# Optimization experiments

Hardware: AMD Instinct MI355X
Metric: run time of the kernel (lower is better)

## Reference

```python
import jax, jax.numpy as jnp
import numpy as np

N = 100000
E = 3200000
IN_DIM = 128
HID = 16
OUT = 2


def setup_inputs() -> dict:
    key = jax.random.key(0)
    k_x, k_e, k_w1, k_w2 = jax.random.split(key, 4)
    x = jax.random.normal(k_x, (N, IN_DIM), dtype=jnp.float32)
    edge_index = jax.random.randint(k_e, (2, E), 0, N, dtype=jnp.int64)
    # Glorot-style init like PyG GCNConv
    W1 = jax.random.normal(k_w1, (IN_DIM, HID), dtype=jnp.float32) * (1.0 / np.sqrt(IN_DIM))
    b1 = jnp.zeros((HID,), dtype=jnp.float32)
    W2 = jax.random.normal(k_w2, (HID, OUT), dtype=jnp.float32) * (1.0 / np.sqrt(HID))
    b2 = jnp.zeros((OUT,), dtype=jnp.float32)
    return {"x": x, "edge_index": edge_index, "W1": W1, "b1": b1, "W2": W2, "b2": b2}


def _gcn_conv(x, src, dst, norm, W, b):
    # PyG GCNConv: linear transform first, then normalized scatter-add, then bias
    h = x @ W                         # [N, out]
    msg = h[src] * norm[:, None]      # gather + per-edge scale
    out = jax.ops.segment_sum(msg, dst, num_segments=N)
    return out + b


def reference(x, edge_index, W1, b1, W2, b2):
    # add self-loops (GCNConv default add_self_loops=True)
    loops = jnp.arange(N, dtype=edge_index.dtype)
    src = jnp.concatenate([edge_index[0], loops])
    dst = jnp.concatenate([edge_index[1], loops])
    # symmetric normalization: deg^{-1/2}[src] * deg^{-1/2}[dst], deg = in-degree incl. self-loops
    deg = jax.ops.segment_sum(jnp.ones_like(dst, dtype=x.dtype), dst, num_segments=N)
    dinv = jnp.where(deg > 0, jax.lax.rsqrt(deg), 0.0)
    norm = dinv[src] * dinv[dst]      # [E + N]

    h = _gcn_conv(x, src, dst, norm, W1, b1)
    h = jax.nn.relu(h)
    h = _gcn_conv(h, src, dst, norm, W2, b2)
    return jax.nn.log_softmax(h, axis=1)
```

## Files before the change

### kernel.cpp

```cpp
#include <hip/hip_runtime.h>

#define N_NODES 100000
#define N_EDGES 3200000
#define IN_DIM  128
#define HID     16
#define OUTC    2

#define NB     256
#define SPAN   391
#define CAP    13250
#define NBLK   800
#define BLK_E  (N_EDGES / NBLK)

__device__ __forceinline__ unsigned short f2b(float f) {
    unsigned u = __float_as_uint(f);
    unsigned r = u + 0x7FFFu + ((u >> 16) & 1u);
    return (unsigned short)(r >> 16);
}
__device__ __forceinline__ float b2f(unsigned short b) {
    return __uint_as_float(((unsigned)b) << 16);
}

__global__ __launch_bounds__(256) void k_count_bb(const int* __restrict__ dst,
                                                  int* __restrict__ bc) {
    __shared__ int h[NB];
    h[threadIdx.x] = 0;
    __syncthreads();
    const int4* d4 = (const int4*)(dst + blockIdx.x * BLK_E);
    for (int i = threadIdx.x; i < BLK_E / 4; i += 256) {
        int4 v = d4[i];
        atomicAdd(&h[(unsigned)v.x / SPAN], 1);
        atomicAdd(&h[(unsigned)v.y / SPAN], 1);
        atomicAdd(&h[(unsigned)v.z / SPAN], 1);
        atomicAdd(&h[(unsigned)v.w / SPAN], 1);
    }
    __syncthreads();
    bc[blockIdx.x * NB + threadIdx.x] = h[threadIdx.x];
}

__global__ __launch_bounds__(256) void k_scan_bb(int* __restrict__ bc,
                                                 int* __restrict__ bcount) {
    __shared__ int s[256];
    int b = blockIdx.x;
    int base = threadIdx.x * 4;
    int vals[4];
    int tsum = 0;
#pragma unroll
    for (int i = 0; i < 4; ++i) {
        int t = base + i;
        vals[i] = (t < NBLK) ? bc[t * NB + b] : 0;
        tsum += vals[i];
    }
    s[threadIdx.x] = tsum;
    __syncthreads();
    for (int ofs = 1; ofs < 256; ofs <<= 1) {
        int u = (threadIdx.x >= ofs) ? s[threadIdx.x - ofs] : 0;
        __syncthreads();
        s[threadIdx.x] += u;
        __syncthreads();
    }
    int run = s[threadIdx.x] - tsum;
#pragma unroll
    for (int i = 0; i < 4; ++i) {
        int t = base + i;
        if (t < NBLK) { bc[t * NB + b] = run; run += vals[i]; }
    }
    if (threadIdx.x == 255) bcount[b] = s[255];
}

__global__ __launch_bounds__(256) void k_fillbkt(const int* __restrict__ src,
                                                 const int* __restrict__ dst,
                                                 const int* __restrict__ bc,
                                                 int2* __restrict__ bpair) {
    __shared__ int h[NB];
    __shared__ int gb[NB];
    h[threadIdx.x] = 0;
    gb[threadIdx.x] = threadIdx.x * CAP + bc[blockIdx.x * NB + threadIdx.x];
    __syncthreads();
    const int4* d4 = (const int4*)(dst + blockIdx.x * BLK_E);
    const int4* s4 = (const int4*)(src + blockIdx.x * BLK_E);
    for (int i = threadIdx.x; i < BLK_E / 4; i += 256) {
        int4 dv = d4[i];
        int4 sv = s4[i];
        int b0 = (unsigned)dv.x / SPAN; int p0 = gb[b0] + atomicAdd(&h[b0], 1); bpair[p0] = make_int2(sv.x, dv.x);
        int b1 = (unsigned)dv.y / SPAN; int p1 = gb[b1] + atomicAdd(&h[b1], 1); bpair[p1] = make_int2(sv.y, dv.y);
        int b2 = (unsigned)dv.z / SPAN; int p2 = gb[b2] + atomicAdd(&h[b2], 1); bpair[p2] = make_int2(sv.z, dv.z);
        int b3 = (unsigned)dv.w / SPAN; int p3 = gb[b3] + atomicAdd(&h[b3], 1); bpair[p3] = make_int2(sv.w, dv.w);
    }
}

__global__ __launch_bounds__(256) void k_build(const int2* __restrict__ bpair,
                                               const int* __restrict__ bcount,
                                               int* __restrict__ cnt,
                                               int* __restrict__ off,
                                               float* __restrict__ dinv,
                                               int* __restrict__ csr) {
    __shared__ int h[SPAN];
    __shared__ int sc[256];
    __shared__ int csrBase;
    int b = blockIdx.x;
    int t = threadIdx.x;

    int bv = bcount[t];
    sc[t] = bv;
    __syncthreads();
    for (int ofs = 1; ofs < 256; ofs <<= 1) {
        int u = (t >= ofs) ? sc[t - ofs] : 0;
        __syncthreads();
        sc[t] += u;
        __syncthreads();
    }
    if (t == b) csrBase = sc[t] - bv;

    for (int i = t; i < SPAN; i += 256) h[i] = 0;
    __syncthreads();

    int tot = bcount[b];
    int base = b * SPAN;
    const int2* bp = bpair + (size_t)b * CAP;

    for (int i = t; i < tot; i += 256)
        atomicAdd(&h[bp[i].y - base], 1);
    __syncthreads();

    int i0 = 2 * t, i1 = 2 * t + 1;
    int c0 = (i0 < SPAN) ? h[i0] : 0;
    int c1 = (i1 < SPAN) ? h[i1] : 0;
    int ts = c0 + c1;
    __syncthreads();
    sc[t] = ts;
    __syncthreads();
    for (int ofs = 1; ofs < 256; ofs <<= 1) {
        int u = (t >= ofs) ? sc[t - ofs] : 0;
        __syncthreads();
        sc[t] += u;
        __syncthreads();
    }
    int ex = sc[t] - ts;
    int g0 = csrBase + ex;
    int g1 = g0 + c0;
    __syncthreads();
    if (i0 < SPAN) {
        int n = base + i0;
        if (n < N_NODES) { cnt[n] = c0; off[n] = g0; dinv[n] = rsqrtf(1.0f + (float)c0); }
        h[i0] = g0;
    }
    if (i1 < SPAN) {
        int n = base + i1;
        if (n < N_NODES) { cnt[n] = c1; off[n] = g1; dinv[n] = rsqrtf(1.0f + (float)c1); }
        h[i1] = g1;
    }
    __syncthreads();

    for (int i = t; i < tot; i += 256) {
        int2 e = bp[i];
        int r = atomicAdd(&h[e.y - base], 1);
        csr[r] = e.x;
    }
}

__global__ __launch_bounds__(256) void k_gemm1(const float* __restrict__ x,
                                               const float* __restrict__ W1,
                                               const float* __restrict__ dinv,
                                               unsigned short* __restrict__ p1b) {
    int n = blockIdx.x * 256 + threadIdx.x;
    if (n >= N_NODES) return;

    float acc[HID];
#pragma unroll
    for (int k = 0; k < HID; ++k) acc[k] = 0.f;

    const float4* xr = (const float4*)(x + (size_t)n * IN_DIM);
#pragma unroll 4
    for (int q = 0; q < IN_DIM / 4; ++q) {
        float4 xv = xr[q];
        const float* wrow = W1 + q * 4 * HID;
#pragma unroll
        for (int k = 0; k < HID; ++k) acc[k] = fmaf(xv.x, wrow[0 * HID + k], acc[k]);
#pragma unroll
        for (int k = 0; k < HID; ++k) acc[k] = fmaf(xv.y, wrow[1 * HID + k], acc[k]);
#pragma unroll
        for (int k = 0; k < HID; ++k) acc[k] = fmaf(xv.z, wrow[2 * HID + k], acc[k]);
#pragma unroll
        for (int k = 0; k < HID; ++k) acc[k] = fmaf(xv.w, wrow[3 * HID + k], acc[k]);
    }

    float di = dinv[n];
    union { unsigned short us[HID]; uint4 v4[2]; } pk;
#pragma unroll
    for (int k = 0; k < HID; ++k) pk.us[k] = f2b(acc[k] * di);
    uint4* op = (uint4*)(p1b + (size_t)n * HID);
    op[0] = pk.v4[0];
    op[1] = pk.v4[1];
}

__global__ __launch_bounds__(256) void k_gather1(const int* __restrict__ csr,
                                                 const int* __restrict__ off,
                                                 const int* __restrict__ cnt,
                                                 const unsigned short* __restrict__ p1b,
                                                 const float* __restrict__ dinv,
                                                 const float* __restrict__ b1,
                                                 const float* __restrict__ W2,
                                                 float* __restrict__ p2b) {
    int gid = blockIdx.x * 256 + threadIdx.x;
    int n = gid >> 4;
    int k = gid & 15;
    if (n >= N_NODES) return;

    int base = off[n];
    int deg = cnt[n];
    float acc = 0.f;
    int j = 0;
    for (; j + 3 < deg; j += 4) {
        int s0 = csr[base + j + 0];
        int s1 = csr[base + j + 1];
        int s2 = csr[base + j + 2];
        int s3 = csr[base + j + 3];
        float v0 = b2f(p1b[s0 * HID + k]);
        float v1 = b2f(p1b[s1 * HID + k]);
        float v2 = b2f(p1b[s2 * HID + k]);
        float v3 = b2f(p1b[s3 * HID + k]);
        acc += (v0 + v1) + (v2 + v3);
    }
    for (; j < deg; ++j) acc += b2f(p1b[csr[base + j] * HID + k]);
    acc += b2f(p1b[n * HID + k]);

    float di = dinv[n];
    float hval = fmaxf(fmaf(di, acc, b1[k]), 0.f);
    float hv = di * hval;
    float t0 = hv * W2[k * OUTC + 0];
    float t1 = hv * W2[k * OUTC + 1];
#pragma unroll
    for (int m = 1; m < HID; m <<= 1) {
        t0 += __shfl_xor(t0, m);
        t1 += __shfl_xor(t1, m);
    }
    if (k == 0) *(float2*)(p2b + n * OUTC) = make_float2(t0, t1);
}

__global__ __launch_bounds__(256) void k_gather2(const int* __restrict__ csr,
                                                 const int* __restrict__ off,
                                                 const int* __restrict__ cnt,
                                                 const float* __restrict__ p2b,
                                                 const float* __restrict__ dinv,
                                                 const float* __restrict__ b2,
                                                 float* __restrict__ out) {
    int gid = blockIdx.x * 256 + threadIdx.x;
    int n = gid >> 4;
    int k = gid & 15;
    if (n >= N_NODES) return;

    int base = off[n];
    int deg = cnt[n];
    float a0 = 0.f, a1 = 0.f;
    for (int j = k; j < deg; j += 16) {
        int s = csr[base + j];
        float2 v = *(const float2*)(p2b + s * OUTC);
        a0 += v.x;
        a1 += v.y;
    }
    if (k == 0) {
        float2 v = *(const float2*)(p2b + n * OUTC);
        a0 += v.x;
        a1 += v.y;
    }
#pragma unroll
    for (int m = 1; m < HID; m <<= 1) {
        a0 += __shfl_xor(a0, m);
        a1 += __shfl_xor(a1, m);
    }
    if (k == 0) {
        float di = dinv[n];
        float v0 = fmaf(di, a0, b2[0]);
        float v1 = fmaf(di, a1, b2[1]);
        float mx = fmaxf(v0, v1);
        float lse = mx + logf(expf(v0 - mx) + expf(v1 - mx));
        *(float2*)(out + n * OUTC) = make_float2(v0 - lse, v1 - lse);
    }
}

extern "C" void kernel_launch(void* const* d_in, const int* in_sizes, int n_in,
                              void* d_out, int out_size, void* d_ws, size_t ws_size,
                              hipStream_t stream) {
    const float* x  = (const float*)d_in[0];
    const int*   ei = (const int*)d_in[1];
    const float* W1 = (const float*)d_in[2];
    const float* b1 = (const float*)d_in[3];
    const float* W2 = (const float*)d_in[4];
    const float* b2 = (const float*)d_in[5];
    float* out = (float*)d_out;

    const int* src = ei;
    const int* dst = ei + N_EDGES;

    int* bc     = (int*)d_ws;
    int* bcount = bc + NBLK * NB;
    int2* bpair = (int2*)(((uintptr_t)(bcount + NB) + 255) & ~(uintptr_t)255);
    int* cnt    = (int*)(bpair + (size_t)NB * CAP);
    int* off    = cnt + N_NODES;
    float* dinv = (float*)(off + N_NODES);
    int* csr    = (int*)(dinv + N_NODES);
    unsigned short* p1b = (unsigned short*)(csr + N_EDGES);
    float* p2b  = (float*)(p1b + (size_t)N_NODES * HID);

    k_count_bb <<<NBLK, 256, 0, stream>>>(dst, bc);
    k_scan_bb  <<<NB, 256, 0, stream>>>(bc, bcount);
    k_fillbkt  <<<NBLK, 256, 0, stream>>>(src, dst, bc, bpair);
    k_build    <<<NB, 256, 0, stream>>>(bpair, bcount, cnt, off, dinv, csr);
    k_gemm1    <<<(N_NODES + 255) / 256, 256, 0, stream>>>(x, W1, dinv, p1b);
    k_gather1  <<<(N_NODES * 16 + 255) / 256, 256, 0, stream>>>(csr, off, cnt, p1b, dinv, b1, W2, p2b);
    k_gather2  <<<(N_NODES * 16 + 255) / 256, 256, 0, stream>>>(csr, off, cnt, p2b, dinv, b2, out);
}
```

Baseline: 143.3 us.

## Pack bucketed edges into 32-bit words and double counting blocks

Bucketed edge pairs are now stored as one 32-bit word: the source index in the low 17 bits and the local destination offset within its bucket in the high bits. This halves the scatter-write and re-read traffic between the fill and build kernels compared with int2 pairs. Separately, the number of edge-partition blocks is doubled to 1600, which raises parallelism in the count and fill kernels. In exchange, the scan kernel now handles 7 values per thread, and the per-block count array becomes larger.

```diff
diff --git a/kernel.cpp b/kernel.cpp
--- a/kernel.cpp
+++ b/kernel.cpp
@@ -9,8 +9,13 @@
 #define NB     256
 #define SPAN   391
 #define CAP    13250
-#define NBLK   800
+#define NBLK   1600
 #define BLK_E  (N_EDGES / NBLK)
+#define VPT    7
+
+#define PACK(s, ld)  ((unsigned)(s) | ((unsigned)(ld) << 17))
+#define P_SRC(p)     ((int)((p) & 0x1FFFFu))
+#define P_LDST(p)    ((int)((p) >> 17))
 
 __device__ __forceinline__ unsigned short f2b(float f) {
     unsigned u = __float_as_uint(f);
@@ -42,11 +47,11 @@
                                                  int* __restrict__ bcount) {
     __shared__ int s[256];
     int b = blockIdx.x;
-    int base = threadIdx.x * 4;
-    int vals[4];
+    int base = threadIdx.x * VPT;
+    int vals[VPT];
     int tsum = 0;
 #pragma unroll
-    for (int i = 0; i < 4; ++i) {
+    for (int i = 0; i < VPT; ++i) {
         int t = base + i;
         vals[i] = (t < NBLK) ? bc[t * NB + b] : 0;
         tsum += vals[i];
@@ -61,7 +66,7 @@
     }
     int run = s[threadIdx.x] - tsum;
 #pragma unroll
-    for (int i = 0; i < 4; ++i) {
+    for (int i = 0; i < VPT; ++i) {
         int t = base + i;
         if (t < NBLK) { bc[t * NB + b] = run; run += vals[i]; }
     }
@@ -71,7 +76,7 @@
 __global__ __launch_bounds__(256) void k_fillbkt(const int* __restrict__ src,
                                                  const int* __restrict__ dst,
                                                  const int* __restrict__ bc,
-                                                 int2* __restrict__ bpair) {
+                                                 unsigned* __restrict__ bpack) {
     __shared__ int h[NB];
     __shared__ int gb[NB];
     h[threadIdx.x] = 0;
@@ -82,14 +87,14 @@
     for (int i = threadIdx.x; i < BLK_E / 4; i += 256) {
         int4 dv = d4[i];
         int4 sv = s4[i];
-        int b0 = (unsigned)dv.x / SPAN; int p0 = gb[b0] + atomicAdd(&h[b0], 1); bpair[p0] = make_int2(sv.x, dv.x);
-        int b1 = (unsigned)dv.y / SPAN; int p1 = gb[b1] + atomicAdd(&h[b1], 1); bpair[p1] = make_int2(sv.y, dv.y);
-        int b2 = (unsigned)dv.z / SPAN; int p2 = gb[b2] + atomicAdd(&h[b2], 1); bpair[p2] = make_int2(sv.z, dv.z);
-        int b3 = (unsigned)dv.w / SPAN; int p3 = gb[b3] + atomicAdd(&h[b3], 1); bpair[p3] = make_int2(sv.w, dv.w);
-    }
-}
-
-__global__ __launch_bounds__(256) void k_build(const int2* __restrict__ bpair,
+        int b0 = (unsigned)dv.x / SPAN; int p0 = gb[b0] + atomicAdd(&h[b0], 1); bpack[p0] = PACK(sv.x, dv.x - b0 * SPAN);
+        int b1 = (unsigned)dv.y / SPAN; int p1 = gb[b1] + atomicAdd(&h[b1], 1); bpack[p1] = PACK(sv.y, dv.y - b1 * SPAN);
+        int b2 = (unsigned)dv.z / SPAN; int p2 = gb[b2] + atomicAdd(&h[b2], 1); bpack[p2] = PACK(sv.z, dv.z - b2 * SPAN);
+        int b3 = (unsigned)dv.w / SPAN; int p3 = gb[b3] + atomicAdd(&h[b3], 1); bpack[p3] = PACK(sv.w, dv.w - b3 * SPAN);
+    }
+}
+
+__global__ __launch_bounds__(256) void k_build(const unsigned* __restrict__ bpack,
                                                const int* __restrict__ bcount,
                                                int* __restrict__ cnt,
                                                int* __restrict__ off,
@@ -116,13 +121,13 @@
     __syncthreads();
 
     int tot = bcount[b];
+    const unsigned* bp = bpack + (size_t)b * CAP;
+
+    for (int i = t; i < tot; i += 256)
+        atomicAdd(&h[P_LDST(bp[i])], 1);
+    __syncthreads();
+
     int base = b * SPAN;
-    const int2* bp = bpair + (size_t)b * CAP;
-
-    for (int i = t; i < tot; i += 256)
-        atomicAdd(&h[bp[i].y - base], 1);
-    __syncthreads();
-
     int i0 = 2 * t, i1 = 2 * t + 1;
     int c0 = (i0 < SPAN) ? h[i0] : 0;
     int c1 = (i1 < SPAN) ? h[i1] : 0;
@@ -153,9 +158,9 @@
     __syncthreads();
 
     for (int i = t; i < tot; i += 256) {
-        int2 e = bp[i];
-        int r = atomicAdd(&h[e.y - base], 1);
-        csr[r] = e.x;
+        unsigned e = bp[i];
+        int r = atomicAdd(&h[P_LDST(e)], 1);
+        csr[r] = P_SRC(e);
     }
 }
 
@@ -295,8 +300,8 @@
 
     int* bc     = (int*)d_ws;
     int* bcount = bc + NBLK * NB;
-    int2* bpair = (int2*)(((uintptr_t)(bcount + NB) + 255) & ~(uintptr_t)255);
-    int* cnt    = (int*)(bpair + (size_t)NB * CAP);
+    unsigned* bpack = (unsigned*)(((uintptr_t)(bcount + NB) + 255) & ~(uintptr_t)255);
+    int* cnt    = (int*)(bpack + (size_t)NB * CAP);
     int* off    = cnt + N_NODES;
     float* dinv = (float*)(off + N_NODES);
     int* csr    = (int*)(dinv + N_NODES);
@@ -305,8 +310,8 @@
 
     k_count_bb <<<NBLK, 256, 0, stream>>>(dst, bc);
     k_scan_bb  <<<NB, 256, 0, stream>>>(bc, bcount);
-    k_fillbkt  <<<NBLK, 256, 0, stream>>>(src, dst, bc, bpair);
-    k_build    <<<NB, 256, 0, stream>>>(bpair, bcount, cnt, off, dinv, csr);
+    k_fillbkt  <<<NBLK, 256, 0, stream>>>(src, dst, bc, bpack);
+    k_build    <<<NB, 256, 0, stream>>>(bpack, bcount, cnt, off, dinv, csr);
     k_gemm1    <<<(N_NODES + 255) / 256, 256, 0, stream>>>(x, W1, dinv, p1b);
     k_gather1  <<<(N_NODES * 16 + 255) / 256, 256, 0, stream>>>(csr, off, cnt, p1b, dinv, b1, W2, p2b);
     k_gather2  <<<(N_NODES * 16 + 255) / 256, 256, 0, stream>>>(csr, off, cnt, p2b, dinv, b2, out);
```

New measurement: 142.4 us. About the same (-0.6%).
